# Performance work log

Hardware: AMD Instinct MI355X
Metric: run time of the kernel (lower is better)

Reference implementation:

```python
import jax, jax.numpy as jnp
import numpy as np

N_HEAD = 16

def setup_inputs() -> dict:
    key = jax.random.key(0)
    ks = jax.random.split(key, 5)
    C = 1024
    x = jax.random.normal(ks[0], (2, 2048, C), dtype=jnp.float32)
    w_attn = jax.random.normal(ks[1], (C, 3 * C), dtype=jnp.float32) * (C ** -0.5)
    b_attn = jax.random.normal(ks[2], (3 * C,), dtype=jnp.float32) * 0.02
    w_proj = jax.random.normal(ks[3], (C, C), dtype=jnp.float32) * (C ** -0.5)
    b_proj = jax.random.normal(ks[4], (C,), dtype=jnp.float32) * 0.02
    return {"x": x, "w_attn": w_attn, "b_attn": b_attn, "w_proj": w_proj, "b_proj": b_proj}

def reference(x, w_attn, b_attn, w_proj, b_proj):
    B, T, C = x.shape
    H = N_HEAD
    D = C // H  # head_dim
    qkv = x @ w_attn + b_attn  # [B,T,3C]
    q, k, v = jnp.split(qkv, 3, axis=-1)
    # [B,T,H,D] -> [B,H,T,D]
    q = q.reshape(B, T, H, D).transpose(0, 2, 1, 3)
    k = k.reshape(B, T, H, D).transpose(0, 2, 1, 3)
    v = v.reshape(B, T, H, D).transpose(0, 2, 1, 3)
    scale = 1.0 / np.sqrt(D).astype(np.float32)
    att = jnp.einsum('bhqd,bhkd->bhqk', q, k) * scale  # [B,H,T,T]
    causal = jnp.tril(jnp.ones((T, T), dtype=bool))
    att = jnp.where(causal, att, jnp.finfo(att.dtype).min)
    att = jax.nn.softmax(att, axis=-1)
    y = jnp.einsum('bhqk,bhkd->bhqd', att, v)  # [B,H,T,D]
    y = y.transpose(0, 2, 1, 3).reshape(B, T, C)
    return y @ w_proj + b_proj
```

## Files before the change

kernel.cpp:

```cpp
#include <hip/hip_runtime.h>
#include <hip/hip_bf16.h>
#include <stdint.h>

typedef __bf16 bf16x8 __attribute__((ext_vector_type(8)));
typedef __bf16 bf16x4 __attribute__((ext_vector_type(4)));
typedef float  f32x4  __attribute__((ext_vector_type(4)));

#define GLOBAL_AS __attribute__((address_space(1)))
#define LDS_AS    __attribute__((address_space(3)))

__device__ __forceinline__ void gld_lds16(const __bf16* g, __bf16* l) {
  __builtin_amdgcn_global_load_lds((GLOBAL_AS void*)g, (LDS_AS void*)l, 16, 0, 0);
}

#define QSCALE 0.18033688011116029f

__device__ __forceinline__ unsigned pk2(float a, float b) {
  unsigned short ua = __builtin_bit_cast(unsigned short, (__bf16)a);
  unsigned short ub = __builtin_bit_cast(unsigned short, (__bf16)b);
  return (unsigned)ua | ((unsigned)ub << 16);
}

union PackU { unsigned u[4]; bf16x8 v; };

__global__ __launch_bounds__(256) void cast_bf16_kernel(const float* __restrict__ src,
                                                        __bf16* __restrict__ dst, int n)
{
  int i = (blockIdx.x * 256 + threadIdx.x) * 8;
  if (i >= n) return;
  float4 a = *(const float4*)(src + i);
  float4 b = *(const float4*)(src + i + 4);
  bf16x8 o;
  o[0]=(__bf16)a.x; o[1]=(__bf16)a.y; o[2]=(__bf16)a.z; o[3]=(__bf16)a.w;
  o[4]=(__bf16)b.x; o[5]=(__bf16)b.y; o[6]=(__bf16)b.z; o[7]=(__bf16)b.w;
  *(bf16x8*)(dst + i) = o;
}

__global__ __launch_bounds__(256) void transpose_cast_kernel(const float* __restrict__ src,
                                                             __bf16* __restrict__ dst,
                                                             int R, int C)
{
  __shared__ float tile[32][33];
  int c0 = blockIdx.x * 32, r0 = blockIdx.y * 32;
  int tx = threadIdx.x & 31, ty = threadIdx.x >> 5;
  #pragma unroll
  for (int i = 0; i < 32; i += 8)
    tile[ty + i][tx] = src[(size_t)(r0 + ty + i) * C + (c0 + tx)];
  __syncthreads();
  #pragma unroll
  for (int i = 0; i < 32; i += 8)
    dst[(size_t)(c0 + ty + i) * R + (r0 + tx)] = (__bf16)tile[tx][ty + i];
}

template<int MODE, int BM>
__global__ __launch_bounds__(256, (BM == 128 ? 3 : 2))
void gemm_kernel(const __bf16* __restrict__ A,
                 const __bf16* __restrict__ Bt,
                 const float*  __restrict__ bias,
                 float* __restrict__ outF,
                 __bf16* __restrict__ qb,
                 __bf16* __restrict__ kb,
                 __bf16* __restrict__ vb,
                 int M, int N, int K)
{
  __shared__ __bf16 As[BM * 64];
  __shared__ __bf16 Bs[128 * 64];
  const int tid  = threadIdx.x;
  const int wave = tid >> 6, lane = tid & 63;
  const int lo = lane & 15, g4 = lane >> 4;
  int bm, bn;
  if (MODE == 0) {
    int bid = blockIdx.x;
    int bm_i = (bid & 7) * 4 + ((bid >> 3) & 3);
    int bn_i = bid >> 5;
    bm = bm_i * 128; bn = bn_i * 128;
  } else {
    bm = blockIdx.y * BM; bn = blockIdx.x * 128;
  }
  const int wr = (wave >> 1) * (BM / 2);
  const int wc = (wave & 1) * 64;
  constexpr int MF = BM / 32;

  f32x4 acc[MF][4] = {};

  const int nkt = K >> 6;
  for (int kt = 0; kt < nkt; ++kt) {
    const int k0 = kt << 6;
    __syncthreads();
    #pragma unroll
    for (int j = 0; j < BM / 32; ++j) {
      int c = j * 256 + tid;
      int r = c >> 3, cc = c & 7;
      int cs = cc ^ (r & 7);
      gld_lds16(A + (size_t)(bm + r) * K + (k0 + cs * 8), As + c * 8);
    }
    #pragma unroll
    for (int j = 0; j < 4; ++j) {
      int c = j * 256 + tid;
      int r = c >> 3, cc = c & 7;
      int cs = cc ^ (r & 7);
      gld_lds16(Bt + (size_t)(bn + r) * K + (k0 + cs * 8), Bs + c * 8);
    }
    __syncthreads();
    #pragma unroll
    for (int ks = 0; ks < 2; ++ks) {
      bf16x8 af[MF], bfr[4];
      #pragma unroll
      for (int mf = 0; mf < MF; ++mf) {
        int row = wr + mf * 16 + lo;
        int ch = (ks * 4 + g4) ^ (row & 7);
        af[mf] = *(const bf16x8*)(As + row * 64 + ch * 8);
      }
      #pragma unroll
      for (int nf = 0; nf < 4; ++nf) {
        int row = wc + nf * 16 + lo;
        int ch = (ks * 4 + g4) ^ (row & 7);
        bfr[nf] = *(const bf16x8*)(Bs + row * 64 + ch * 8);
      }
      #pragma unroll
      for (int mf = 0; mf < MF; ++mf)
        #pragma unroll
        for (int nf = 0; nf < 4; ++nf)
          acc[mf][nf] = __builtin_amdgcn_mfma_f32_16x16x32_bf16(af[mf], bfr[nf], acc[mf][nf], 0, 0, 0);
    }
  }

  float bv[4];
  #pragma unroll
  for (int nf = 0; nf < 4; ++nf) bv[nf] = bias[bn + wc + nf * 16 + lo];

  if (MODE == 1) {
    #pragma unroll
    for (int mf = 0; mf < MF; ++mf)
      #pragma unroll
      for (int nf = 0; nf < 4; ++nf) {
        int col = bn + wc + nf * 16 + lo;
        #pragma unroll
        for (int j = 0; j < 4; ++j) {
          int row = bm + wr + mf * 16 + g4 * 4 + j;
          outF[(size_t)row * N + col] = acc[mf][nf][j] + bv[nf];
        }
      }
  } else {
    #pragma unroll
    for (int mf = 0; mf < MF; ++mf) {
      const int tbase = bm + wr + mf * 16 + g4 * 4;
      const int b = tbase >> 11, t = tbase & 2047;
      #pragma unroll
      for (int nf = 0; nf < 4; ++nf) {
        int n = bn + wc + nf * 16 + lo;
        int sel = n >> 10, hd = n & 1023;
        int h = hd >> 6, d = hd & 63;
        size_t bh = (size_t)(b * 16 + h);
        if (sel == 2) {
          bf16x4 pv;
          #pragma unroll
          for (int j = 0; j < 4; ++j) pv[j] = (__bf16)(acc[mf][nf][j] + bv[nf]);
          *(bf16x4*)(vb + (bh * 64 + d) * 2048 + t) = pv;
        } else if (sel == 0) {
          #pragma unroll
          for (int j = 0; j < 4; ++j)
            qb[(bh * 2048 + (size_t)(t + j)) * 64 + d] = (__bf16)((acc[mf][nf][j] + bv[nf]) * QSCALE);
        } else {
          #pragma unroll
          for (int j = 0; j < 4; ++j)
            kb[(bh * 2048 + (size_t)(t + j)) * 64 + d] = (__bf16)(acc[mf][nf][j] + bv[nf]);
        }
      }
    }
  }
}

__global__ __launch_bounds__(256, 4)
void attn_kernel(const __bf16* __restrict__ qg_, const __bf16* __restrict__ kg,
                 const __bf16* __restrict__ vg, __bf16* __restrict__ yg,
                 __bf16* __restrict__ pY, float* __restrict__ pL)
{
  const int n = blockIdx.x;
  const int xcd = n & 7;
  const int m = n >> 3;
  const int bh = xcd + 8 * (m & 3);
  const int t = m >> 2;
  const int b = bh >> 4, h = bh & 15;

  const int tid  = threadIdx.x;
  const int wave = tid >> 6;
  const int lane = tid & 63;
  const int l15  = lane & 15;
  const int g    = lane >> 4;
  const int sw   = l15 & 7;

  __shared__ __bf16 Kb[2][64 * 64];
  __shared__ __bf16 Vb[2][64 * 64];

  const __bf16* qbase = qg_ + (size_t)bh * 2048 * 64;
  const __bf16* kbase = kg  + (size_t)bh * 2048 * 64;
  const __bf16* vbase = vg  + (size_t)bh * 64 * 2048;

  bf16x8 qf0, qf1;
  f32x4 o0, o1, o2, o3, osum;

  bf16x8 ones;
  #pragma unroll
  for (int j = 0; j < 8; ++j) ones[j] = (__bf16)1.0f;

  auto LOADQ = [&](int strip) {
    const int q16 = strip * 64 + wave * 16 + l15;
    qf0 = *(const bf16x8*)(qbase + (size_t)q16 * 64 + g * 8);
    qf1 = *(const bf16x8*)(qbase + (size_t)q16 * 64 + 32 + g * 8);
  };
  auto RESET = [&]() {
    o0 = f32x4{}; o1 = f32x4{}; o2 = f32x4{}; o3 = f32x4{}; osum = f32x4{};
  };
  auto STAGE = [&](int kt, int bsel) {
    #pragma unroll
    for (int j = 0; j < 2; ++j) {
      int c = j * 256 + tid;
      int cr = c >> 3, cc = c & 7;
      int cs = cc ^ (cr & 7);
      int pr = (cr & 0x23) | ((cr & 0x10) >> 2) | ((cr & 0x0C) << 1);
      gld_lds16(kbase + (size_t)(kt * 64 + pr) * 64 + cs * 8, &Kb[bsel][0] + c * 8);
      gld_lds16(vbase + (size_t)cr * 2048 + (kt * 64 + cs * 8), &Vb[bsel][0] + c * 8);
    }
  };

  auto TILE = [&](int cur, bool diag) {
    const __bf16* KL = &Kb[cur][0];
    f32x4 s0 = {}, s1 = {}, s2 = {}, s3 = {};
    {
      bf16x8 k00 = *(const bf16x8*)(KL + (0  + l15) * 64 + ((0 + g) ^ sw) * 8);
      bf16x8 k01 = *(const bf16x8*)(KL + (0  + l15) * 64 + ((4 + g) ^ sw) * 8);
      bf16x8 k10 = *(const bf16x8*)(KL + (16 + l15) * 64 + ((0 + g) ^ sw) * 8);
      bf16x8 k11 = *(const bf16x8*)(KL + (16 + l15) * 64 + ((4 + g) ^ sw) * 8);
      bf16x8 k20 = *(const bf16x8*)(KL + (32 + l15) * 64 + ((0 + g) ^ sw) * 8);
      bf16x8 k21 = *(const bf16x8*)(KL + (32 + l15) * 64 + ((4 + g) ^ sw) * 8);
      bf16x8 k30 = *(const bf16x8*)(KL + (48 + l15) * 64 + ((0 + g) ^ sw) * 8);
      bf16x8 k31 = *(const bf16x8*)(KL + (48 + l15) * 64 + ((4 + g) ^ sw) * 8);
      __builtin_amdgcn_s_setprio(1);
      s0 = __builtin_amdgcn_mfma_f32_16x16x32_bf16(k00, qf0, s0, 0, 0, 0);
      s0 = __builtin_amdgcn_mfma_f32_16x16x32_bf16(k01, qf1, s0, 0, 0, 0);
      s1 = __builtin_amdgcn_mfma_f32_16x16x32_bf16(k10, qf0, s1, 0, 0, 0);
      s1 = __builtin_amdgcn_mfma_f32_16x16x32_bf16(k11, qf1, s1, 0, 0, 0);
      s2 = __builtin_amdgcn_mfma_f32_16x16x32_bf16(k20, qf0, s2, 0, 0, 0);
      s2 = __builtin_amdgcn_mfma_f32_16x16x32_bf16(k21, qf1, s2, 0, 0, 0);
      s3 = __builtin_amdgcn_mfma_f32_16x16x32_bf16(k30, qf0, s3, 0, 0, 0);
      s3 = __builtin_amdgcn_mfma_f32_16x16x32_bf16(k31, qf1, s3, 0, 0, 0);
      __builtin_amdgcn_s_setprio(0);
    }

    if (diag) {
      const int qr = wave * 16 + l15;
      #pragma unroll
      for (int r2 = 0; r2 < 4; ++r2) {
        if (8 * g + r2          > qr) s0[r2] = -3.0e38f;
        if (8 * g + 4 + r2      > qr) s1[r2] = -3.0e38f;
        if (32 + 8 * g + r2     > qr) s2[r2] = -3.0e38f;
        if (32 + 8 * g + 4 + r2 > qr) s3[r2] = -3.0e38f;
      }
    }

    #pragma unroll
    for (int r2 = 0; r2 < 4; ++r2) s0[r2] = exp2f(s0[r2]);
    #pragma unroll
    for (int r2 = 0; r2 < 4; ++r2) s1[r2] = exp2f(s1[r2]);
    #pragma unroll
    for (int r2 = 0; r2 < 4; ++r2) s2[r2] = exp2f(s2[r2]);
    #pragma unroll
    for (int r2 = 0; r2 < 4; ++r2) s3[r2] = exp2f(s3[r2]);

    PackU pa0, pa1;
    pa0.u[0] = pk2(s0[0], s0[1]); pa0.u[1] = pk2(s0[2], s0[3]);
    pa0.u[2] = pk2(s1[0], s1[1]); pa0.u[3] = pk2(s1[2], s1[3]);
    pa1.u[0] = pk2(s2[0], s2[1]); pa1.u[1] = pk2(s2[2], s2[3]);
    pa1.u[2] = pk2(s3[0], s3[1]); pa1.u[3] = pk2(s3[2], s3[3]);

    const __bf16* VL = &Vb[cur][0];
    bf16x8 v00 = *(const bf16x8*)(VL + (0  + l15) * 64 + ((0 + g) ^ sw) * 8);
    bf16x8 v01 = *(const bf16x8*)(VL + (0  + l15) * 64 + ((4 + g) ^ sw) * 8);
    bf16x8 v10 = *(const bf16x8*)(VL + (16 + l15) * 64 + ((0 + g) ^ sw) * 8);
    bf16x8 v11 = *(const bf16x8*)(VL + (16 + l15) * 64 + ((4 + g) ^ sw) * 8);
    bf16x8 v20 = *(const bf16x8*)(VL + (32 + l15) * 64 + ((0 + g) ^ sw) * 8);
    bf16x8 v21 = *(const bf16x8*)(VL + (32 + l15) * 64 + ((4 + g) ^ sw) * 8);
    bf16x8 v30 = *(const bf16x8*)(VL + (48 + l15) * 64 + ((0 + g) ^ sw) * 8);
    bf16x8 v31 = *(const bf16x8*)(VL + (48 + l15) * 64 + ((4 + g) ^ sw) * 8);

    __builtin_amdgcn_s_setprio(1);
    osum = __builtin_amdgcn_mfma_f32_16x16x32_bf16(pa0.v, ones, osum, 0, 0, 0);
    osum = __builtin_amdgcn_mfma_f32_16x16x32_bf16(pa1.v, ones, osum, 0, 0, 0);
    o0 = __builtin_amdgcn_mfma_f32_16x16x32_bf16(pa0.v, v00, o0, 0, 0, 0);
    o0 = __builtin_amdgcn_mfma_f32_16x16x32_bf16(pa1.v, v01, o0, 0, 0, 0);
    o1 = __builtin_amdgcn_mfma_f32_16x16x32_bf16(pa0.v, v10, o1, 0, 0, 0);
    o1 = __builtin_amdgcn_mfma_f32_16x16x32_bf16(pa1.v, v11, o1, 0, 0, 0);
    o2 = __builtin_amdgcn_mfma_f32_16x16x32_bf16(pa0.v, v20, o2, 0, 0, 0);
    o2 = __builtin_amdgcn_mfma_f32_16x16x32_bf16(pa1.v, v21, o2, 0, 0, 0);
    o3 = __builtin_amdgcn_mfma_f32_16x16x32_bf16(pa0.v, v30, o3, 0, 0, 0);
    o3 = __builtin_amdgcn_mfma_f32_16x16x32_bf16(pa1.v, v31, o3, 0, 0, 0);
    __builtin_amdgcn_s_setprio(0);
  };

  auto WRITE_Y = [&](int strip) {
    #pragma unroll
    for (int r2 = 0; r2 < 4; ++r2) {
      float il = 1.0f / osum[r2];
      int trow = strip * 64 + wave * 16 + 4 * g + r2;
      __bf16* dst = yg + ((size_t)(b * 2048 + trow)) * 1024 + h * 64;
      dst[l15]      = (__bf16)(o0[r2] * il);
      dst[16 + l15] = (__bf16)(o1[r2] * il);
      dst[32 + l15] = (__bf16)(o2[r2] * il);
      dst[48 + l15] = (__bf16)(o3[r2] * il);
    }
  };
  auto WRITE_PART = [&](int slot) {
    __bf16* po = pY + (size_t)slot * 4096;
    #pragma unroll
    for (int r2 = 0; r2 < 4; ++r2) {
      int row = wave * 16 + 4 * g + r2;
      __bf16* dst = po + row * 64;
      dst[l15]      = (__bf16)o0[r2];
      dst[16 + l15] = (__bf16)o1[r2];
      dst[32 + l15] = (__bf16)o2[r2];
      dst[48 + l15] = (__bf16)o3[r2];
    }
    if (l15 == 0) {
      #pragma unroll
      for (int r2 = 0; r2 < 4; ++r2)
        pL[slot * 64 + wave * 16 + 4 * g + r2] = osum[r2];
    }
  };

  int cur = 0;
  if (t < 16) {
    LOADQ(t); RESET();
    bf16x8 qB0, qB1;
    {
      const int q16b = (31 - t) * 64 + wave * 16 + l15;
      qB0 = *(const bf16x8*)(qbase + (size_t)q16b * 64 + g * 8);
      qB1 = *(const bf16x8*)(qbase + (size_t)q16b * 64 + 32 + g * 8);
    }
    STAGE(0, 0);
    for (int j = 0; j < 17; ++j) {
      __syncthreads();
      if (j < 16) {
        int nx = j + 1;
        STAGE((nx <= t) ? nx : (nx + 15 - t), cur ^ 1);
      }
      if (j <= t) {
        TILE(cur, j == t);
        if (j == t) { WRITE_Y(t); qf0 = qB0; qf1 = qB1; RESET(); }
      } else {
        TILE(cur, j == 16);
      }
      cur ^= 1;
    }
    WRITE_PART((bh * 16 + (15 - t)) * 2 + 1);
  } else {
    LOADQ(t); RESET();
    STAGE(0, 0);
    for (int j = 0; j < 16; ++j) {
      __syncthreads();
      if (j < 15) STAGE(j + 1, cur ^ 1);
      TILE(cur, false);
      cur ^= 1;
    }
    WRITE_PART((bh * 16 + (t - 16)) * 2);
  }
}

__global__ __launch_bounds__(256)
void attn_merge_kernel(const __bf16* __restrict__ pY, const float* __restrict__ pL,
                       __bf16* __restrict__ yg)
{
  const int us = blockIdx.x & 15, bh = blockIdx.x >> 4;
  const int b = bh >> 4, h = bh & 15;
  const int tid = threadIdx.x;
  const int row = tid >> 2, d0 = (tid & 3) * 16;
  const int slotA = (bh * 16 + us) * 2, slotB = slotA + 1;

  float l = pL[slotA * 64 + row] + pL[slotB * 64 + row];
  float inv = 1.0f / l;

  const __bf16* pa = pY + (size_t)slotA * 4096 + row * 64 + d0;
  const __bf16* pb = pY + (size_t)slotB * 4096 + row * 64 + d0;
  __bf16* dst = yg + ((size_t)(b * 2048 + (16 + us) * 64 + row)) * 1024 + h * 64 + d0;

  bf16x8 a0 = *(const bf16x8*)pa, a1 = *(const bf16x8*)(pa + 8);
  bf16x8 b0 = *(const bf16x8*)pb, b1 = *(const bf16x8*)(pb + 8);
  bf16x8 r0, r1;
  #pragma unroll
  for (int j = 0; j < 8; ++j) {
    r0[j] = (__bf16)(((float)a0[j] + (float)b0[j]) * inv);
    r1[j] = (__bf16)(((float)a1[j] + (float)b1[j]) * inv);
  }
  *(bf16x8*)dst = r0;
  *(bf16x8*)(dst + 8) = r1;
}

extern "C" void kernel_launch(void* const* d_in, const int* in_sizes, int n_in,
                              void* d_out, int out_size, void* d_ws, size_t ws_size,
                              hipStream_t stream)
{
  const float* x      = (const float*)d_in[0];
  const float* w_attn = (const float*)d_in[1];
  const float* b_attn = (const float*)d_in[2];
  const float* w_proj = (const float*)d_in[3];
  const float* b_proj = (const float*)d_in[4];
  float* out = (float*)d_out;

  __bf16* xb  = (__bf16*)d_ws;
  __bf16* waT = xb  + (size_t)4096 * 1024;
  __bf16* wpT = waT + (size_t)3072 * 1024;
  __bf16* qb  = wpT + (size_t)1024 * 1024;
  __bf16* kb  = qb  + (size_t)32 * 2048 * 64;
  __bf16* vb  = kb  + (size_t)32 * 2048 * 64;
  __bf16* yb  = vb  + (size_t)32 * 2048 * 64;

  __bf16* pY = xb;
  float*  pL = (float*)waT;

  cast_bf16_kernel<<<2048, 256, 0, stream>>>(x, xb, 4096 * 1024);
  transpose_cast_kernel<<<dim3(96, 32), 256, 0, stream>>>(w_attn, waT, 1024, 3072);
  transpose_cast_kernel<<<dim3(32, 32), 256, 0, stream>>>(w_proj, wpT, 1024, 1024);
  gemm_kernel<0, 128><<<768, 256, 0, stream>>>(xb, waT, b_attn, nullptr,
                                               qb, kb, vb, 4096, 3072, 1024);
  attn_kernel<<<1024, 256, 0, stream>>>(qb, kb, vb, yb, pY, pL);
  attn_merge_kernel<<<512, 256, 0, stream>>>(pY, pL, yb);
  gemm_kernel<1, 64><<<dim3(8, 64), 256, 0, stream>>>(yb, wpT, b_proj, out,
                                                      nullptr, nullptr, nullptr, 4096, 1024, 1024);
}
```

Measured before the change: 99.88 us.

## Merge prep kernels into one launch and switch GEMM to 32x32x16 MFMA

Merges the input cast and the two weight transpose-casts into a single prep kernel, which removes two kernel launches and their inter-kernel gaps. Separately, the GEMM inner loop moves from 16x16x32 to 32x32x16 bf16 MFMA tiles. Each wave now issues fewer, larger MFMAs and does fewer LDS fragment loads per unit of compute. The epilogue index mapping is rewritten for the 32x32 accumulator layout, with some risk of mapping errors and a changed store access pattern.

```diff
diff --git a/kernel.cpp b/kernel.cpp
--- a/kernel.cpp
+++ b/kernel.cpp
@@ -5,6 +5,7 @@
 typedef __bf16 bf16x8 __attribute__((ext_vector_type(8)));
 typedef __bf16 bf16x4 __attribute__((ext_vector_type(4)));
 typedef float  f32x4  __attribute__((ext_vector_type(4)));
+typedef float  f32x16 __attribute__((ext_vector_type(16)));
 
 #define GLOBAL_AS __attribute__((address_space(1)))
 #define LDS_AS    __attribute__((address_space(3)))
@@ -23,26 +24,35 @@
 
 union PackU { unsigned u[4]; bf16x8 v; };
 
-__global__ __launch_bounds__(256) void cast_bf16_kernel(const float* __restrict__ src,
-                                                        __bf16* __restrict__ dst, int n)
+__global__ __launch_bounds__(256)
+void prep_kernel(const float* __restrict__ x, __bf16* __restrict__ xb,
+                 const float* __restrict__ wa, __bf16* __restrict__ waT,
+                 const float* __restrict__ wp, __bf16* __restrict__ wpT)
 {
-  int i = (blockIdx.x * 256 + threadIdx.x) * 8;
-  if (i >= n) return;
-  float4 a = *(const float4*)(src + i);
-  float4 b = *(const float4*)(src + i + 4);
-  bf16x8 o;
-  o[0]=(__bf16)a.x; o[1]=(__bf16)a.y; o[2]=(__bf16)a.z; o[3]=(__bf16)a.w;
-  o[4]=(__bf16)b.x; o[5]=(__bf16)b.y; o[6]=(__bf16)b.z; o[7]=(__bf16)b.w;
-  *(bf16x8*)(dst + i) = o;
-}
-
-__global__ __launch_bounds__(256) void transpose_cast_kernel(const float* __restrict__ src,
-                                                             __bf16* __restrict__ dst,
-                                                             int R, int C)
-{
+  const int id = blockIdx.x;
+  const int tid = threadIdx.x;
+  if (id < 2048) {
+    int i = (id * 256 + tid) * 8;
+    float4 a = *(const float4*)(x + i);
+    float4 b = *(const float4*)(x + i + 4);
+    bf16x8 o;
+    o[0]=(__bf16)a.x; o[1]=(__bf16)a.y; o[2]=(__bf16)a.z; o[3]=(__bf16)a.w;
+    o[4]=(__bf16)b.x; o[5]=(__bf16)b.y; o[6]=(__bf16)b.z; o[7]=(__bf16)b.w;
+    *(bf16x8*)(xb + i) = o;
+    return;
+  }
   __shared__ float tile[32][33];
-  int c0 = blockIdx.x * 32, r0 = blockIdx.y * 32;
-  int tx = threadIdx.x & 31, ty = threadIdx.x >> 5;
+  const float* src; __bf16* dst; int R, C, c0, r0;
+  if (id < 5120) {
+    int idx = id - 2048;
+    src = wa; dst = waT; R = 1024; C = 3072;
+    c0 = (idx % 96) * 32; r0 = (idx / 96) * 32;
+  } else {
+    int idx = id - 5120;
+    src = wp; dst = wpT; R = 1024; C = 1024;
+    c0 = (idx & 31) * 32; r0 = (idx >> 5) * 32;
+  }
+  int tx = tid & 31, ty = tid >> 5;
   #pragma unroll
   for (int i = 0; i < 32; i += 8)
     tile[ty + i][tx] = src[(size_t)(r0 + ty + i) * C + (c0 + tx)];
@@ -67,7 +77,7 @@
   __shared__ __bf16 Bs[128 * 64];
   const int tid  = threadIdx.x;
   const int wave = tid >> 6, lane = tid & 63;
-  const int lo = lane & 15, g4 = lane >> 4;
+  const int l31 = lane & 31, hi = lane >> 5;
   int bm, bn;
   if (MODE == 0) {
     int bid = blockIdx.x;
@@ -79,9 +89,9 @@
   }
   const int wr = (wave >> 1) * (BM / 2);
   const int wc = (wave & 1) * 64;
-  constexpr int MF = BM / 32;
-
-  f32x4 acc[MF][4] = {};
+  constexpr int MT = BM / 64;
+
+  f32x16 acc[MT][2] = {};
 
   const int nkt = K >> 6;
   for (int kt = 0; kt < nkt; ++kt) {
@@ -103,68 +113,75 @@
     }
     __syncthreads();
     #pragma unroll
-    for (int ks = 0; ks < 2; ++ks) {
-      bf16x8 af[MF], bfr[4];
-      #pragma unroll
-      for (int mf = 0; mf < MF; ++mf) {
-        int row = wr + mf * 16 + lo;
-        int ch = (ks * 4 + g4) ^ (row & 7);
-        af[mf] = *(const bf16x8*)(As + row * 64 + ch * 8);
-      }
-      #pragma unroll
-      for (int nf = 0; nf < 4; ++nf) {
-        int row = wc + nf * 16 + lo;
-        int ch = (ks * 4 + g4) ^ (row & 7);
-        bfr[nf] = *(const bf16x8*)(Bs + row * 64 + ch * 8);
-      }
-      #pragma unroll
-      for (int mf = 0; mf < MF; ++mf)
+    for (int kk = 0; kk < 4; ++kk) {
+      bf16x8 af[MT], bfr[2];
+      #pragma unroll
+      for (int mt = 0; mt < MT; ++mt) {
+        int row = wr + mt * 32 + l31;
+        int ch = (kk * 2 + hi) ^ (row & 7);
+        af[mt] = *(const bf16x8*)(As + row * 64 + ch * 8);
+      }
+      #pragma unroll
+      for (int nt = 0; nt < 2; ++nt) {
+        int row = wc + nt * 32 + l31;
+        int ch = (kk * 2 + hi) ^ (row & 7);
+        bfr[nt] = *(const bf16x8*)(Bs + row * 64 + ch * 8);
+      }
+      #pragma unroll
+      for (int mt = 0; mt < MT; ++mt)
         #pragma unroll
-        for (int nf = 0; nf < 4; ++nf)
-          acc[mf][nf] = __builtin_amdgcn_mfma_f32_16x16x32_bf16(af[mf], bfr[nf], acc[mf][nf], 0, 0, 0);
-    }
-  }
-
-  float bv[4];
+        for (int nt = 0; nt < 2; ++nt)
+          acc[mt][nt] = __builtin_amdgcn_mfma_f32_32x32x16_bf16(af[mt], bfr[nt], acc[mt][nt], 0, 0, 0);
+    }
+  }
+
+  float bv[2];
   #pragma unroll
-  for (int nf = 0; nf < 4; ++nf) bv[nf] = bias[bn + wc + nf * 16 + lo];
+  for (int nt = 0; nt < 2; ++nt) bv[nt] = bias[bn + wc + nt * 32 + l31];
 
   if (MODE == 1) {
     #pragma unroll
-    for (int mf = 0; mf < MF; ++mf)
-      #pragma unroll
-      for (int nf = 0; nf < 4; ++nf) {
-        int col = bn + wc + nf * 16 + lo;
+    for (int mt = 0; mt < MT; ++mt)
+      #pragma unroll
+      for (int nt = 0; nt < 2; ++nt) {
+        int col = bn + wc + nt * 32 + l31;
         #pragma unroll
-        for (int j = 0; j < 4; ++j) {
-          int row = bm + wr + mf * 16 + g4 * 4 + j;
-          outF[(size_t)row * N + col] = acc[mf][nf][j] + bv[nf];
-        }
-      }
-  } else {
-    #pragma unroll
-    for (int mf = 0; mf < MF; ++mf) {
-      const int tbase = bm + wr + mf * 16 + g4 * 4;
-      const int b = tbase >> 11, t = tbase & 2047;
-      #pragma unroll
-      for (int nf = 0; nf < 4; ++nf) {
-        int n = bn + wc + nf * 16 + lo;
-        int sel = n >> 10, hd = n & 1023;
-        int h = hd >> 6, d = hd & 63;
-        size_t bh = (size_t)(b * 16 + h);
-        if (sel == 2) {
-          bf16x4 pv;
-          #pragma unroll
-          for (int j = 0; j < 4; ++j) pv[j] = (__bf16)(acc[mf][nf][j] + bv[nf]);
-          *(bf16x4*)(vb + (bh * 64 + d) * 2048 + t) = pv;
-        } else if (sel == 0) {
+        for (int q2 = 0; q2 < 4; ++q2) {
+          int rbase = bm + wr + mt * 32 + 8 * q2 + 4 * hi;
           #pragma unroll
           for (int j = 0; j < 4; ++j)
-            qb[(bh * 2048 + (size_t)(t + j)) * 64 + d] = (__bf16)((acc[mf][nf][j] + bv[nf]) * QSCALE);
-        } else {
-          #pragma unroll
-          for (int j = 0; j < 4; ++j)
-            kb[(bh * 2048 + (size_t)(t + j)) * 64 + d] = (__bf16)(acc[mf][nf][j] + bv[nf]);
+            outF[(size_t)(rbase + j) * N + col] = acc[mt][nt][q2 * 4 + j] + bv[nt];
+        }
+      }
+  } else {
+    #pragma unroll
+    for (int mt = 0; mt < MT; ++mt) {
+      #pragma unroll
+      for (int q2 = 0; q2 < 4; ++q2) {
+        const int tbase = bm + wr + mt * 32 + 8 * q2 + 4 * hi;
+        const int b = tbase >> 11, t = tbase & 2047;
+        #pragma unroll
+        for (int nt = 0; nt < 2; ++nt) {
+          int n = bn + wc + nt * 32 + l31;
+          int sel = n >> 10, hd = n & 1023;
+          int h = hd >> 6, d = hd & 63;
+          size_t bh = (size_t)(b * 16 + h);
+          if (sel == 2) {
+            bf16x4 pv;
+            #pragma unroll
+            for (int j = 0; j < 4; ++j) pv[j] = (__bf16)(acc[mt][nt][q2 * 4 + j] + bv[nt]);
+            *(bf16x4*)(vb + (bh * 64 + d) * 2048 + t) = pv;
+          } else if (sel == 0) {
+            #pragma unroll
+            for (int j = 0; j < 4; ++j)
+              qb[(bh * 2048 + (size_t)(t + j)) * 64 + d] =
+                  (__bf16)((acc[mt][nt][q2 * 4 + j] + bv[nt]) * QSCALE);
+          } else {
+            #pragma unroll
+            for (int j = 0; j < 4; ++j)
+              kb[(bh * 2048 + (size_t)(t + j)) * 64 + d] =
+                  (__bf16)(acc[mt][nt][q2 * 4 + j] + bv[nt]);
+          }
         }
       }
     }
@@ -417,9 +434,7 @@
   __bf16* pY = xb;
   float*  pL = (float*)waT;
 
-  cast_bf16_kernel<<<2048, 256, 0, stream>>>(x, xb, 4096 * 1024);
-  transpose_cast_kernel<<<dim3(96, 32), 256, 0, stream>>>(w_attn, waT, 1024, 3072);
-  transpose_cast_kernel<<<dim3(32, 32), 256, 0, stream>>>(w_proj, wpT, 1024, 1024);
+  prep_kernel<<<6144, 256, 0, stream>>>(x, xb, w_attn, waT, w_proj, wpT);
   gemm_kernel<0, 128><<<768, 256, 0, stream>>>(xb, waT, b_attn, nullptr,
                                                qb, kb, vb, 4096, 3072, 1024);
   attn_kernel<<<1024, 256, 0, stream>>>(qb, kb, vb, yb, pY, pL);
```

Measured after the change: 100.0 us. Within noise of the previous version (+0.1%).
